# Performance work log

Measured on AMD Instinct MI355X. Metric: run time of the kernel, lower is better.

The kernel has to match this reference:

```python
import jax, jax.numpy as jnp
import numpy as np

K_PRESERVED = 384   # num_preserved_tokens
NUM_HEADS = 6       # config.num_attention_heads // 2


def setup_inputs() -> dict:
    key = jax.random.key(0)
    ks = jax.random.split(key, 10)
    B, L, D, H = 16, 512, 768, 12
    U = D // 2  # num_units of the router attention
    s = 0.02
    return {
        "hidden_states": jax.random.normal(ks[0], (B, L, D), jnp.float32),
        "self_attention_scores": jax.random.uniform(ks[1], (B, H, L, L), jnp.float32),
        "Wq": jax.random.normal(ks[2], (D, U), jnp.float32) * s,
        "bq": jnp.zeros((U,), jnp.float32),
        "Wk": jax.random.normal(ks[3], (D, U), jnp.float32) * s,
        "bk": jnp.zeros((U,), jnp.float32),
        "Wv": jax.random.normal(ks[4], (D, U), jnp.float32) * s,
        "bv": jnp.zeros((U,), jnp.float32),
        "Wo": jax.random.normal(ks[5], (U, D), jnp.float32) * s,
        "bo": jnp.zeros((D,), jnp.float32),
    }


def _forward(hidden_states, self_attention_scores, Wq, bq, Wk, bk, Wv, bv, Wo, bo):
    B, L, D = hidden_states.shape
    K = K_PRESERVED
    r = L - K  # number of tokens merged away by ToMe
    batch_idx = jnp.arange(B)[:, None]

    class_token = hidden_states[:, :1, :]

    # importance = column sums of head-averaged attention with zeroed diagonal (detached)
    s = jax.lax.stop_gradient(jnp.mean(self_attention_scores, axis=1))  # [B,L,L]
    s = s * (1.0 - jnp.eye(L, dtype=s.dtype))
    importance = jnp.sum(s, axis=1)  # [B,L]
    _, important_idx = jax.lax.top_k(importance, K)  # [B,K]
    important_mask = jnp.zeros((B, L), bool).at[batch_idx, important_idx].set(True)

    # --- ToMe bipartite_soft_matching(hidden_states, r), mode='mean' ---
    metric = jax.lax.stop_gradient(hidden_states)
    metric = metric / jnp.linalg.norm(metric, axis=-1, keepdims=True)
    a, b = metric[:, ::2, :], metric[:, 1::2, :]            # [B,L/2,D] each
    sim = jnp.einsum('bid,bjd->bij', a, b)                   # [B,L/2,L/2]
    node_max = jnp.max(sim, axis=-1)                         # [B,L/2]
    node_idx = jnp.argmax(sim, axis=-1)                      # [B,L/2]
    edge_idx = jnp.argsort(-node_max, axis=-1)               # descending
    src_idx = edge_idx[:, :r]                                # merged src tokens
    unm_idx = edge_idx[:, r:]                                # unmerged src tokens
    dst_idx = jnp.take_along_axis(node_idx, src_idx, axis=1)  # [B,r]

    src_x = hidden_states[:, ::2, :]
    dst_x = hidden_states[:, 1::2, :]                        # [B,L/2,D]
    unm = jnp.take_along_axis(src_x, unm_idx[..., None], axis=1)   # [B,L/2-r,D]
    src_sel = jnp.take_along_axis(src_x, src_idx[..., None], axis=1)  # [B,r,D]
    # scatter_reduce(mean, include_self=True): (dst + sum srcs) / (1 + count)
    sums = dst_x.at[batch_idx, dst_idx].add(src_sel)
    counts = jnp.ones((B, L // 2), dst_x.dtype).at[batch_idx, dst_idx].add(1.0)
    dst_merged = sums / counts[..., None]
    preserved_tokens = jnp.concatenate([unm, dst_merged], axis=1)  # [B,K,D]

    # attention_mask is None -> sentences is the first token
    sentences = hidden_states[:, :1, :]

    # unpreserved tokens: boolean-mask gather, preserving original order
    order = jnp.argsort(important_mask.astype(jnp.int32), axis=1, stable=True)
    unp_idx = order[:, : L - K]                              # [B,L-K]
    unpreserved = hidden_states[batch_idx, unp_idx]          # [B,L-K,D]

    # router multi-head attention: query=sentence, key/value=unpreserved
    U = Wq.shape[1]
    hd = U // NUM_HEADS
    q = (sentences @ Wq + bq).reshape(B, 1, NUM_HEADS, hd)
    k = (unpreserved @ Wk + bk).reshape(B, L - K, NUM_HEADS, hd)
    v = (unpreserved @ Wv + bv).reshape(B, L - K, NUM_HEADS, hd)
    att = jax.nn.softmax(jnp.einsum('bqhd,bkhd->bhqk', q, k) / jnp.sqrt(jnp.asarray(hd, q.dtype)), axis=-1)
    ctx = jnp.einsum('bhqk,bkhd->bqhd', att, v).reshape(B, 1, U)
    new_token = ctx @ Wo + bo                                # [B,1,D]

    final_token = jnp.concatenate([class_token, preserved_tokens, new_token], axis=1)  # [B,K+2,D]
    return final_token


def reference(hidden_states, self_attention_scores, Wq, bq, Wk, bk, Wv, bv, Wo, bo):
    return _forward(hidden_states, self_attention_scores, Wq, bq, Wk, bk, Wv, bv, Wo, bo)
```

## Files before the change

### kernel.cpp

```cpp
#include <hip/hip_runtime.h>
#include <hip/hip_bf16.h>

#define BB 16
#define LL 512
#define DD 768
#define NHEAD 12
#define HALF 256
#define KPRES 384
#define RCNT 128
#define UDIM 384
#define NH2 6
#define HD 64

__device__ float              g_colsum_part[BB * NHEAD * 4 * LL];
__device__ unsigned long long g_nodep_part[BB * HALF * 4];
__device__ int                g_unm[BB * RCNT];
__device__ int                g_srctok[BB * RCNT];
__device__ int                g_srcdst[BB * RCNT];
__device__ int                g_unp[BB * RCNT];
__device__ float              g_ctx[BB * UDIM];

__global__ void k_colsum(const float* __restrict__ sc) {
    int blk = blockIdx.x;
    int ic = blk & 3;
    int bh = blk >> 2;
    int j4 = threadIdx.x;
    const float* base = sc + (size_t)bh * LL * LL;
    int i0 = ic * 128;
    float ax = 0.f, ay = 0.f, az = 0.f, aw = 0.f;
    for (int i = 0; i < 128; i++) {
        float4 v = ((const float4*)(base + (size_t)(i0 + i) * LL))[j4];
        ax += v.x; ay += v.y; az += v.z; aw += v.w;
    }
#pragma unroll
    for (int c = 0; c < 4; c++) {
        int cj = 4 * j4 + c;
        if (cj >= i0 && cj < i0 + 128) {
            float d = base[(size_t)cj * LL + cj];
            if (c == 0) ax -= d; else if (c == 1) ay -= d;
            else if (c == 2) az -= d; else aw -= d;
        }
    }
    float* o = &g_colsum_part[(size_t)blk * LL + 4 * j4];
    o[0] = ax; o[1] = ay; o[2] = az; o[3] = aw;
}

__global__ void k_metric(const float* __restrict__ hs, float* __restrict__ metric) {
    int row = blockIdx.x;
    int t = threadIdx.x;
    __shared__ float red[256];
    const float* src = hs + (size_t)row * DD;
    float v0 = src[t], v1 = src[t + 256], v2 = src[t + 512];
    red[t] = ((0.f + v0 * v0) + v1 * v1) + v2 * v2;
    __syncthreads();
    for (int s = 128; s > 0; s >>= 1) {
        if (t < s) red[t] += red[t + s];
        __syncthreads();
    }
    float nrm = sqrtf(red[0]);
    float* dst = metric + (size_t)row * DD;
    dst[t] = v0 / nrm; dst[t + 256] = v1 / nrm; dst[t + 512] = v2 / nrm;
}

__global__ void k_sim(const float* __restrict__ metric) {
    int b = blockIdx.x, it = blockIdx.y, jt = blockIdx.z;
    int i0 = it * 64, j0 = jt * 64;
    __shared__ float As[64][20];
    __shared__ float BsT[16][68];
    __shared__ unsigned long long cand[64][16];
    int t  = threadIdx.x;
    int ti = t >> 4, tj = t & 15;
    float acc[4][4];
#pragma unroll
    for (int a = 0; a < 4; a++)
#pragma unroll
        for (int c = 0; c < 4; c++) acc[a][c] = 0.f;
    const float* mb = metric + (size_t)b * LL * DD;
    int sr = t >> 2, sc4 = t & 3;
    const float* arow = mb + (size_t)(2 * (i0 + sr)) * DD;
    const float* brow = mb + (size_t)(2 * (j0 + sr) + 1) * DD;
    float4 a4 = ((const float4*)arow)[sc4];
    float4 b4 = ((const float4*)brow)[sc4];
    for (int s = 0; s < 48; s++) {
        __syncthreads();
        *(float4*)&As[sr][4 * sc4] = a4;
        BsT[4 * sc4 + 0][sr] = b4.x;
        BsT[4 * sc4 + 1][sr] = b4.y;
        BsT[4 * sc4 + 2][sr] = b4.z;
        BsT[4 * sc4 + 3][sr] = b4.w;
        __syncthreads();
        if (s + 1 < 48) {
            int d0 = (s + 1) * 16;
            a4 = ((const float4*)(arow + d0))[sc4];
            b4 = ((const float4*)(brow + d0))[sc4];
        }
#pragma unroll
        for (int c4 = 0; c4 < 4; c4++) {
            float4 av[4], bk4[4];
#pragma unroll
            for (int a = 0; a < 4; a++) av[a] = *(const float4*)&As[ti * 4 + a][4 * c4];
#pragma unroll
            for (int k = 0; k < 4; k++) bk4[k] = *(const float4*)&BsT[4 * c4 + k][4 * tj];
#pragma unroll
            for (int k = 0; k < 4; k++) {
#pragma unroll
                for (int a = 0; a < 4; a++) {
                    float ak = ((const float*)&av[a])[k];
#pragma unroll
                    for (int c = 0; c < 4; c++)
                        acc[a][c] += ak * ((const float*)&bk4[k])[c];
                }
            }
        }
    }
#pragma unroll
    for (int a = 0; a < 4; a++) {
        unsigned long long bp = 0ULL;
#pragma unroll
        for (int c = 0; c < 4; c++) {
            int jg = j0 + tj * 4 + c;
            unsigned u = __float_as_uint(acc[a][c]);
            u = (u & 0x80000000u) ? ~u : (u | 0x80000000u);
            unsigned long long p = ((unsigned long long)u << 32) | (unsigned long long)(255 - jg);
            if (p > bp) bp = p;
        }
        cand[ti * 4 + a][tj] = bp;
    }
    __syncthreads();
    if (t < 64) {
        unsigned long long m = cand[t][0];
#pragma unroll
        for (int c2 = 1; c2 < 16; c2++) { unsigned long long v = cand[t][c2]; if (v > m) m = v; }
        g_nodep_part[((size_t)b * HALF + i0 + t) * 4 + jt] = m;
    }
}

__global__ void k_seledge(int* dummy) {
    int b = blockIdx.x, t = threadIdx.x;
    __shared__ float v[LL];
    __shared__ int pos[LL];
    __shared__ float nm[HALF];
    __shared__ int   ni[HALF];
    float imp = 0.f;
    for (int p = 0; p < NHEAD * 4; p++)
        imp += g_colsum_part[((size_t)b * NHEAD * 4 + p) * LL + t];
    v[t] = imp;
    __syncthreads();
    int cnt = 0;
    for (int k = 0; k < LL; k++) {
        float vk = v[k];
        cnt += (vk > imp) || (vk == imp && k < t);
    }
    int notp = (cnt >= KPRES) ? 1 : 0;
    pos[t] = notp;
    __syncthreads();
    for (int s = 1; s < LL; s <<= 1) {
        int add = (t >= s) ? pos[t - s] : 0;
        __syncthreads();
        pos[t] += add;
        __syncthreads();
    }
    if (notp) g_unp[b * RCNT + pos[t] - 1] = t;
    if (t < HALF) {
        unsigned long long p = g_nodep_part[((size_t)b * HALF + t) * 4 + 0];
#pragma unroll
        for (int q = 1; q < 4; q++) {
            unsigned long long w = g_nodep_part[((size_t)b * HALF + t) * 4 + q];
            if (w > p) p = w;
        }
        unsigned u = (unsigned)(p >> 32);
        unsigned bits = (u & 0x80000000u) ? (u & 0x7FFFFFFFu) : ~u;
        nm[t] = __uint_as_float(bits);
        ni[t] = 255 - (int)(p & 0xFFFFFFFFu);
    }
    __syncthreads();
    if (t < HALF) {
        float vv = nm[t];
        int cnt2 = 0;
        for (int k = 0; k < HALF; k++) {
            float vk = nm[k];
            cnt2 += (vk > vv) || (vk == vv && k < t);
        }
        if (cnt2 < RCNT) {
            g_srctok[b * RCNT + cnt2] = t;
            g_srcdst[b * RCNT + cnt2] = ni[t];
        } else {
            g_unm[b * RCNT + (cnt2 - RCNT)] = 2 * t;
        }
    }
}

__global__ void k_attn(const float* __restrict__ hs,
                       const float* __restrict__ Wq, const float* __restrict__ bq,
                       const float* __restrict__ Wk, const float* __restrict__ bk,
                       const float* __restrict__ Wv, const float* __restrict__ bv) {
    int h = blockIdx.x % NH2, b = blockIdx.x / NH2;
    int t = threadIdx.x;
    __shared__ float h0[DD];
    __shared__ float wk2[DD];
    __shared__ float hbar[DD];
    __shared__ float qs[HD];
    __shared__ float red[256];
    __shared__ float att[RCNT];
    __shared__ int   toks[RCNT];
    __shared__ float qbk;
    const float* hb = hs + (size_t)b * LL * DD;
    for (int d = t; d < DD; d += 256) h0[d] = hb[d];
    if (t < RCNT) toks[t] = g_unp[b * RCNT + t];
    __syncthreads();
    {
        int u = t & 63, part = t >> 6;
        float a = 0.f;
        for (int d = part * 192; d < part * 192 + 192; d++)
            a += h0[d] * Wq[(size_t)d * UDIM + h * HD + u];
        red[t] = a;
        __syncthreads();
        if (t < HD)
            qs[t] = bq[h * HD + t] + red[t] + red[t + 64] + red[t + 128] + red[t + 192];
        __syncthreads();
    }
    for (int d = t; d < DD; d += 256) {
        const float4* wrow = (const float4*)(Wk + (size_t)d * UDIM + h * HD);
        const float4* q4 = (const float4*)qs;
        float4 s4 = {0.f, 0.f, 0.f, 0.f};
#pragma unroll
        for (int u4 = 0; u4 < 16; u4++) {
            float4 w = wrow[u4], q = q4[u4];
            s4.x += q.x * w.x; s4.y += q.y * w.y; s4.z += q.z * w.z; s4.w += q.w * w.w;
        }
        wk2[d] = (s4.x + s4.y) + (s4.z + s4.w);
    }
    if (t == 0) {
        float a = 0.f;
        for (int u = 0; u < HD; u++) a += qs[u] * bk[h * HD + u];
        qbk = a;
    }
    __syncthreads();
    {
        int tok = t >> 1, half = t & 1;
        const float4* hr4 = (const float4*)(hb + (size_t)toks[tok] * DD) + half * 96;
        const float4* wk4 = (const float4*)wk2 + half * 96;
        float4 s4 = {0.f, 0.f, 0.f, 0.f};
        for (int d4 = 0; d4 < 96; d4++) {
            float4 w = wk4[d4], x = hr4[d4];
            s4.x += w.x * x.x; s4.y += w.y * x.y; s4.z += w.z * x.z; s4.w += w.w * x.w;
        }
        red[t] = (s4.x + s4.y) + (s4.z + s4.w);
    }
    __syncthreads();
    float lg = -1e30f;
    if (t < RCNT) lg = (qbk + red[2 * t] + red[2 * t + 1]) * 0.125f;
    __syncthreads();
    red[t] = lg;
    __syncthreads();
    for (int s = 128; s > 0; s >>= 1) {
        if (t < s) red[t] = fmaxf(red[t], red[t + s]);
        __syncthreads();
    }
    float mx = red[0];
    __syncthreads();
    float e = (t < RCNT) ? expf(lg - mx) : 0.f;
    red[t] = e;
    __syncthreads();
    for (int s = 128; s > 0; s >>= 1) {
        if (t < s) red[t] += red[t + s];
        __syncthreads();
    }
    float inv = 1.f / red[0];
    __syncthreads();
    if (t < RCNT) att[t] = e * inv;
    __syncthreads();
    if (t < DD / 4) {
        float4 a4 = {0.f, 0.f, 0.f, 0.f};
        for (int s2 = 0; s2 < RCNT; s2++) {
            float w = att[s2];
            float4 x = ((const float4*)(hb + (size_t)toks[s2] * DD))[t];
            a4.x += w * x.x; a4.y += w * x.y; a4.z += w * x.z; a4.w += w * x.w;
        }
        *(float4*)&hbar[4 * t] = a4;
    }
    __syncthreads();
    {
        int u = t & 63, part = t >> 6;
        float a = 0.f;
        for (int d = part * 192; d < part * 192 + 192; d++)
            a += hbar[d] * Wv[(size_t)d * UDIM + h * HD + u];
        red[t] = a;
        __syncthreads();
        if (t < HD)
            g_ctx[b * UDIM + h * HD + t] =
                bv[h * HD + t] + red[t] + red[t + 64] + red[t + 128] + red[t + 192];
    }
}

__global__ void k_rows(const float* __restrict__ hs,
                       const float* __restrict__ Wo, const float* __restrict__ bo,
                       float* __restrict__ out) {
    int blk = blockIdx.x;
    int t = threadIdx.x;
    if (blk < BB * 385) {
        int row = blk % 385, b = blk / 385;
        float4* o4 = (float4*)(out + ((size_t)b * 386 + row) * DD);
        if (row == 0) {
            const float4* s4 = (const float4*)(hs + (size_t)b * LL * DD);
            o4[t] = s4[t];
        } else if (row <= RCNT) {
            int tok = g_unm[b * RCNT + row - 1];
            const float4* s4 = (const float4*)(hs + ((size_t)b * LL + tok) * DD);
            o4[t] = s4[t];
        } else {
            int j = row - 1 - RCNT;
            __shared__ int ss[RCNT], sd[RCNT];
            if (t < RCNT) { ss[t] = g_srctok[b * RCNT + t]; sd[t] = g_srcdst[b * RCNT + t]; }
            __syncthreads();
            float4 acc = ((const float4*)(hs + ((size_t)b * LL + 2 * j + 1) * DD))[t];
            float cnt = 1.f;
            for (int s2 = 0; s2 < RCNT; s2++) {
                if (sd[s2] == j) {
                    float4 v = ((const float4*)(hs + ((size_t)b * LL + 2 * ss[s2]) * DD))[t];
                    acc.x += v.x; acc.y += v.y; acc.z += v.z; acc.w += v.w;
                    cnt += 1.f;
                }
            }
            float4 r; r.x = acc.x / cnt; r.y = acc.y / cnt; r.z = acc.z / cnt; r.w = acc.w / cnt;
            o4[t] = r;
        }
    } else {
        int b = blk - BB * 385;
        __shared__ float c[UDIM];
        c[t] = g_ctx[b * UDIM + t];
        c[t + 192] = g_ctx[b * UDIM + t + 192];
        __syncthreads();
#pragma unroll
        for (int kk = 0; kk < 4; kk++) {
            int dd = t + 192 * kk;
            float acc = bo[dd];
            for (int u = 0; u < UDIM; u++)
                acc += c[u] * Wo[(size_t)u * DD + dd];
            out[((size_t)b * 386 + 385) * DD + dd] = acc;
        }
    }
}

extern "C" void kernel_launch(void* const* d_in, const int* in_sizes, int n_in,
                              void* d_out, int out_size, void* d_ws, size_t ws_size,
                              hipStream_t stream) {
    const float* hs = (const float*)d_in[0];
    const float* sc = (const float*)d_in[1];
    const float* Wq = (const float*)d_in[2];
    const float* bq = (const float*)d_in[3];
    const float* Wk = (const float*)d_in[4];
    const float* bk = (const float*)d_in[5];
    const float* Wv = (const float*)d_in[6];
    const float* bv = (const float*)d_in[7];
    const float* Wo = (const float*)d_in[8];
    const float* bo = (const float*)d_in[9];
    float* out = (float*)d_out;
    float* metric = (float*)d_ws;

    k_colsum<<<BB * NHEAD * 4, 128, 0, stream>>>(sc);
    k_metric<<<BB * LL, 256, 0, stream>>>(hs, metric);
    k_sim<<<dim3(BB, 4, 4), 256, 0, stream>>>(metric);
    k_seledge<<<BB, 512, 0, stream>>>(nullptr);
    k_attn<<<BB * NH2, 256, 0, stream>>>(hs, Wq, bq, Wk, bk, Wv, bv);
    k_rows<<<BB * 385 + BB, 192, 0, stream>>>(hs, Wo, bo, out);
}
```

Baseline: 527.9 us.

## Fuse column-sum and norm kernels; normalize on the fly in similarity GEMM

```diff
diff --git a/kernel.cpp b/kernel.cpp
--- a/kernel.cpp
+++ b/kernel.cpp
@@ -13,6 +13,7 @@
 #define HD 64
 
 __device__ float              g_colsum_part[BB * NHEAD * 4 * LL];
+__device__ float              g_norms[BB * LL];
 __device__ unsigned long long g_nodep_part[BB * HALF * 4];
 __device__ int                g_unm[BB * RCNT];
 __device__ int                g_srctok[BB * RCNT];
@@ -20,67 +21,70 @@
 __device__ int                g_unp[BB * RCNT];
 __device__ float              g_ctx[BB * UDIM];
 
-__global__ void k_colsum(const float* __restrict__ sc) {
+__global__ void k_colnorm(const float* __restrict__ sc, const float* __restrict__ hs) {
     int blk = blockIdx.x;
-    int ic = blk & 3;
-    int bh = blk >> 2;
-    int j4 = threadIdx.x;
-    const float* base = sc + (size_t)bh * LL * LL;
-    int i0 = ic * 128;
-    float ax = 0.f, ay = 0.f, az = 0.f, aw = 0.f;
-    for (int i = 0; i < 128; i++) {
-        float4 v = ((const float4*)(base + (size_t)(i0 + i) * LL))[j4];
-        ax += v.x; ay += v.y; az += v.z; aw += v.w;
-    }
-#pragma unroll
-    for (int c = 0; c < 4; c++) {
-        int cj = 4 * j4 + c;
-        if (cj >= i0 && cj < i0 + 128) {
-            float d = base[(size_t)cj * LL + cj];
-            if (c == 0) ax -= d; else if (c == 1) ay -= d;
-            else if (c == 2) az -= d; else aw -= d;
-        }
-    }
-    float* o = &g_colsum_part[(size_t)blk * LL + 4 * j4];
-    o[0] = ax; o[1] = ay; o[2] = az; o[3] = aw;
-}
-
-__global__ void k_metric(const float* __restrict__ hs, float* __restrict__ metric) {
-    int row = blockIdx.x;
     int t = threadIdx.x;
     __shared__ float red[256];
-    const float* src = hs + (size_t)row * DD;
-    float v0 = src[t], v1 = src[t + 256], v2 = src[t + 512];
-    red[t] = ((0.f + v0 * v0) + v1 * v1) + v2 * v2;
-    __syncthreads();
-    for (int s = 128; s > 0; s >>= 1) {
-        if (t < s) red[t] += red[t + s];
-        __syncthreads();
-    }
-    float nrm = sqrtf(red[0]);
-    float* dst = metric + (size_t)row * DD;
-    dst[t] = v0 / nrm; dst[t + 256] = v1 / nrm; dst[t + 512] = v2 / nrm;
-}
-
-__global__ void k_sim(const float* __restrict__ metric) {
+    if (blk < BB * NHEAD * 4) {
+        int ic = blk & 3;
+        int bh = blk >> 2;
+        const float* base = sc + (size_t)bh * LL * LL;
+        int i0 = ic * 128;
+        float ax = 0.f, ay = 0.f;
+        for (int i = 0; i < 128; i++) {
+            float2 v = ((const float2*)(base + (size_t)(i0 + i) * LL))[t];
+            ax += v.x; ay += v.y;
+        }
+#pragma unroll
+        for (int c = 0; c < 2; c++) {
+            int cj = 2 * t + c;
+            if (cj >= i0 && cj < i0 + 128) {
+                float d = base[(size_t)cj * LL + cj];
+                if (c == 0) ax -= d; else ay -= d;
+            }
+        }
+        g_colsum_part[(size_t)blk * LL + 2 * t] = ax;
+        g_colsum_part[(size_t)blk * LL + 2 * t + 1] = ay;
+    } else {
+        int row = blk - BB * NHEAD * 4;
+        const float* src = hs + (size_t)row * DD;
+        float v0 = src[t], v1 = src[t + 256], v2 = src[t + 512];
+        red[t] = ((0.f + v0 * v0) + v1 * v1) + v2 * v2;
+        __syncthreads();
+        for (int s = 128; s > 0; s >>= 1) {
+            if (t < s) red[t] += red[t + s];
+            __syncthreads();
+        }
+        if (t == 0) g_norms[row] = sqrtf(red[0]);
+    }
+}
+
+__global__ void k_sim(const float* __restrict__ hs) {
     int b = blockIdx.x, it = blockIdx.y, jt = blockIdx.z;
     int i0 = it * 64, j0 = jt * 64;
     __shared__ float As[64][20];
     __shared__ float BsT[16][68];
+    __shared__ float nA[64], nB[64];
     __shared__ unsigned long long cand[64][16];
     int t  = threadIdx.x;
     int ti = t >> 4, tj = t & 15;
+    if (t < 64) nA[t] = g_norms[b * LL + 2 * (i0 + t)];
+    else if (t < 128) nB[t - 64] = g_norms[b * LL + 2 * (j0 + t - 64) + 1];
     float acc[4][4];
 #pragma unroll
     for (int a = 0; a < 4; a++)
 #pragma unroll
         for (int c = 0; c < 4; c++) acc[a][c] = 0.f;
-    const float* mb = metric + (size_t)b * LL * DD;
+    const float* hb = hs + (size_t)b * LL * DD;
     int sr = t >> 2, sc4 = t & 3;
-    const float* arow = mb + (size_t)(2 * (i0 + sr)) * DD;
-    const float* brow = mb + (size_t)(2 * (j0 + sr) + 1) * DD;
+    const float* arow = hb + (size_t)(2 * (i0 + sr)) * DD;
+    const float* brow = hb + (size_t)(2 * (j0 + sr) + 1) * DD;
+    __syncthreads();
+    float inA = nA[sr], inB = nB[sr];
     float4 a4 = ((const float4*)arow)[sc4];
     float4 b4 = ((const float4*)brow)[sc4];
+    a4.x /= inA; a4.y /= inA; a4.z /= inA; a4.w /= inA;
+    b4.x /= inB; b4.y /= inB; b4.z /= inB; b4.w /= inB;
     for (int s = 0; s < 48; s++) {
         __syncthreads();
         *(float4*)&As[sr][4 * sc4] = a4;
@@ -93,6 +97,8 @@
             int d0 = (s + 1) * 16;
             a4 = ((const float4*)(arow + d0))[sc4];
             b4 = ((const float4*)(brow + d0))[sc4];
+            a4.x /= inA; a4.y /= inA; a4.z /= inA; a4.w /= inA;
+            b4.x /= inB; b4.y /= inB; b4.z /= inB; b4.w /= inB;
         }
 #pragma unroll
         for (int c4 = 0; c4 < 4; c4++) {
@@ -356,11 +362,10 @@
     const float* Wo = (const float*)d_in[8];
     const float* bo = (const float*)d_in[9];
     float* out = (float*)d_out;
-    float* metric = (float*)d_ws;
-
-    k_colsum<<<BB * NHEAD * 4, 128, 0, stream>>>(sc);
-    k_metric<<<BB * LL, 256, 0, stream>>>(hs, metric);
-    k_sim<<<dim3(BB, 4, 4), 256, 0, stream>>>(metric);
+    (void)d_ws; (void)ws_size;
+
+    k_colnorm<<<BB * NHEAD * 4 + BB * LL, 256, 0, stream>>>(sc, hs);
+    k_sim<<<dim3(BB, 4, 4), 256, 0, stream>>>(hs);
     k_seledge<<<BB, 512, 0, stream>>>(nullptr);
     k_attn<<<BB * NH2, 256, 0, stream>>>(hs, Wq, bq, Wk, bk, Wv, bv);
     k_rows<<<BB * 385 + BB, 192, 0, stream>>>(hs, Wo, bo, out);
```

Result: no change. 521.9 us (-1.1%).
